# Performance work log

Measured on AMD Instinct MI355X. Metric: run time of the kernel, lower is better.

## Reference

```python
import jax, jax.numpy as jnp
import numpy as np

N = 1048576      # obstacle points
E = 16           # polytope half-planes
HID = 32         # MLP hidden width
J = 10           # unrolled PDHG steps
TAU = 0.5
SIGMA = 0.5
RES = 0.5        # residual_scale for learned prox


def setup_inputs() -> dict:
    key = jax.random.key(0)
    ks = jax.random.split(key, 8)
    f32 = jnp.float32
    x = jax.random.normal(ks[0], (N, 2), dtype=f32) * 3.0
    # geometry buffers: regular 16-gon half-planes G mu <= h
    ang = np.arange(E) * (2.0 * np.pi / E)
    G = jnp.asarray(np.stack([np.cos(ang), np.sin(ang)], axis=1), dtype=f32)  # [E,2]
    h = jnp.ones((E, 1), dtype=f32)
    # encoder: Linear(2->HID), Linear(HID->HID)
    W1 = jax.random.normal(ks[1], (2, HID), dtype=f32) * 0.5
    b1 = jnp.zeros((HID,), dtype=f32)
    W2 = jax.random.normal(ks[2], (HID, HID), dtype=f32) * 0.2
    b2 = jnp.zeros((HID,), dtype=f32)
    # init_mu: Linear(HID->E); init_y: Linear(HID->2)
    Wmu = jax.random.normal(ks[3], (HID, E), dtype=f32) * 0.2
    bmu = jnp.zeros((E,), dtype=f32)
    Wy = jax.random.normal(ks[4], (HID, 2), dtype=f32) * 0.2
    by = jnp.zeros((2,), dtype=f32)
    # prox_head: Linear(2->HID) -> ReLU -> Linear(HID->E)
    Wp1 = jax.random.normal(ks[5], (2, HID), dtype=f32) * 0.5
    bp1 = jnp.zeros((HID,), dtype=f32)
    Wp2 = jax.random.normal(ks[6], (HID, E), dtype=f32) * 0.2
    bp2 = jnp.zeros((E,), dtype=f32)
    return dict(x=x, G=G, h=h, W1=W1, b1=b1, W2=W2, b2=b2,
                Wmu=Wmu, bmu=bmu, Wy=Wy, by=by,
                Wp1=Wp1, bp1=bp1, Wp2=Wp2, bp2=bp2)


def reference(x, G, h, W1, b1, W2, b2, Wmu, bmu, Wy, by, Wp1, bp1, Wp2, bp2):
    def project_mu(mu):
        # clamp_min(0), then scale rows so ||mu @ G||_2 <= 1
        mu = jnp.maximum(mu, 0.0)
        vn = jnp.linalg.norm(mu @ G, axis=1, keepdims=True)  # [N,1]
        return mu / jnp.maximum(vn, 1.0)

    feats = jax.nn.relu(x @ W1 + b1)
    feats = jax.nn.relu(feats @ W2 + b2)
    mu = jax.nn.relu(feats @ Wmu + bmu)          # [N,E]
    y = jnp.tanh(feats @ Wy + by)                # [N,2]
    a_row = x @ G.T - h.T                        # [N,E], constant across steps

    def step(carry, _):
        y, mu = carry
        # dual ascent + unit-ball projection on y
        y = y + SIGMA * (mu @ G)
        y = y / jnp.maximum(jnp.linalg.norm(y, axis=1, keepdims=True), 1.0)
        # primal update on mu
        mu = mu + TAU * (a_row - y @ G.T)
        # learned prox correction
        z = mu @ G                                # [N,2]
        delta = jax.nn.relu(z @ Wp1 + bp1) @ Wp2 + bp2
        mu = project_mu(mu + RES * delta)
        return (y, mu), None

    (y, mu), _ = jax.lax.scan(step, (y, mu), None, length=J)
    return project_mu(mu)
```

## Files before the change

kernel.cpp:

```cpp
#include <hip/hip_runtime.h>

#define E 16
#define HID 32
#define NSTEP 10
#define TAU 0.5f
#define SIGMA 0.5f
#define RES 0.5f
#define NT 4
#define STRIDE 36

typedef __attribute__((ext_vector_type(8))) short bf16x8;
typedef __attribute__((ext_vector_type(4))) float f32x4;
typedef __attribute__((ext_vector_type(4))) unsigned int u32x4;

__device__ __forceinline__ f32x4 mfma16(bf16x8 a, bf16x8 b, f32x4 c) {
    return __builtin_amdgcn_mfma_f32_16x16x32_bf16(a, b, c, 0, 0, 0);
}
__device__ __forceinline__ unsigned int pk2(float lo, float hi) {
    unsigned int r;
    asm("v_cvt_pk_bf16_f32 %0, %1, %2" : "=v"(r) : "v"(lo), "v"(hi));
    return r;
}
__device__ __forceinline__ void split8(const float v[8], bf16x8& hi, bf16x8& lo) {
    u32x4 H, L;
#pragma unroll
    for (int j = 0; j < 4; ++j) {
        const unsigned int h = pk2(v[2 * j], v[2 * j + 1]);
        H[j] = h;
        const float h0 = __uint_as_float(h << 16);
        const float h1 = __uint_as_float(h & 0xffff0000u);
        L[j] = pk2(v[2 * j] - h0, v[2 * j + 1] - h1);
    }
    hi = __builtin_bit_cast(bf16x8, H);
    lo = __builtin_bit_cast(bf16x8, L);
}

__device__ __forceinline__ float fast_tanh(float v) {
    float e = __expf(2.0f * v);
    return 1.0f - __fdividef(2.0f, e + 1.0f);
}
__device__ __forceinline__ float inv_norm_clamped(float n2) {
    return fminf(__builtin_amdgcn_rsqf(n2), 1.0f);
}
__device__ __forceinline__ float bsum4(float x) {
    x += __shfl_xor(x, 16);
    x += __shfl_xor(x, 32);
    return x;
}

__global__ __attribute__((amdgpu_waves_per_eu(3, 4))) __launch_bounds__(256)
void pdhg_kernel(
    const float* __restrict__ xg,  const float* __restrict__ Gg,  const float* __restrict__ hg,
    const float* __restrict__ W1,  const float* __restrict__ b1,
    const float* __restrict__ W2,  const float* __restrict__ b2,
    const float* __restrict__ Wmu, const float* __restrict__ bmu,
    const float* __restrict__ Wy,  const float* __restrict__ by,
    const float* __restrict__ Wp1, const float* __restrict__ bp1,
    const float* __restrict__ Wp2, const float* __restrict__ bp2,
    float* __restrict__ out, int npts)
{
    __shared__ __align__(16) float sT[256 * STRIDE];
    const int tid = threadIdx.x;

    {
        const int pt = blockIdx.x * 256 + tid;
        const int ptc = min(pt, npts - 1);
        const float2 xv = reinterpret_cast<const float2*>(xg)[ptc];
        const float x0 = xv.x, x1 = xv.y;

        float g[HID];
        #pragma unroll
        for (int j = 0; j < HID; ++j) g[j] = b2[j];
        #pragma unroll
        for (int ci = 0; ci < 4; ++ci) {
            float fc[8];
            #pragma unroll
            for (int jj = 0; jj < 8; ++jj) {
                const int j = ci * 8 + jj;
                fc[jj] = fmaxf(fmaf(x0, W1[j], fmaf(x1, W1[HID + j], b1[j])), 0.0f);
            }
            #pragma unroll
            for (int ii = 0; ii < 8; ++ii) {
                const int i = ci * 8 + ii;
                #pragma unroll
                for (int j = 0; j < HID; ++j) g[j] = fmaf(fc[ii], W2[i * HID + j], g[j]);
            }
        }
        float* row = sT + tid * STRIDE;
        row[0] = x0; row[1] = x1;
        #pragma unroll
        for (int jq = 0; jq < 8; ++jq) {
            const int j = jq * 4;
            reinterpret_cast<float4*>(row + 4)[jq] = make_float4(
                fmaxf(g[j], 0.f), fmaxf(g[j + 1], 0.f),
                fmaxf(g[j + 2], 0.f), fmaxf(g[j + 3], 0.f));
        }
    }
    __syncthreads();

    const int lane = tid & 63;
    const int colq = lane & 15;
    const int kg   = lane >> 4;
    const int k0   = kg * 8;
    const int e0   = kg * 4;
    const int pbase = blockIdx.x * 256 + (tid >> 6) * 64;

    float gxr[4], gyr[4];
    f32x4 bp2c;
    #pragma unroll
    for (int r = 0; r < 4; ++r) {
        gxr[r] = Gg[2 * (e0 + r)];
        gyr[r] = Gg[2 * (e0 + r) + 1];
        bp2c[r] = bp2[e0 + r];
    }
    float tg00, tg01, tg11;
    {
        float s00 = 0.f, s01 = 0.f, s11 = 0.f;
        #pragma unroll
        for (int r = 0; r < 4; ++r) {
            s00 = fmaf(gxr[r], gxr[r], s00);
            s01 = fmaf(gxr[r], gyr[r], s01);
            s11 = fmaf(gyr[r], gyr[r], s11);
        }
        tg00 = TAU * bsum4(s00);
        tg01 = TAU * bsum4(s01);
        tg11 = TAU * bsum4(s11);
    }

    bf16x8 wp2h, wp2l;
    {
        float w[8];
        #pragma unroll
        for (int i = 0; i < 8; ++i) w[i] = Wp2[(k0 + i) * E + colq];
        split8(w, wp2h, wp2l);
    }
    float wp1a[8], wp1b[8], bp1r[8];
    #pragma unroll
    for (int i = 0; i < 8; ++i) {
        wp1a[i] = Wp1[k0 + i];
        wp1b[i] = Wp1[HID + k0 + i];
        bp1r[i] = bp1[k0 + i];
    }

    float mu[NT][4], ta[NT][4];
    float y0[NT], y1[NT], v0[NT], v1[NT], tc0[NT], tc1[NT];

    {
        bf16x8 wmuh, wmul;
        {
            float w[8];
            #pragma unroll
            for (int i = 0; i < 8; ++i) w[i] = Wmu[(k0 + i) * E + colq];
            split8(w, wmuh, wmul);
        }
        f32x4 bmuc;
        float hr[4];
        #pragma unroll
        for (int r = 0; r < 4; ++r) { bmuc[r] = bmu[e0 + r]; hr[r] = hg[e0 + r]; }
        float wyar[8], wybr[8];
        #pragma unroll
        for (int i = 0; i < 8; ++i) {
            wyar[i] = Wy[(k0 + i) * 2];
            wybr[i] = Wy[(k0 + i) * 2 + 1];
        }
        const float by0 = by[0], by1 = by[1];

        #pragma unroll
        for (int t = 0; t < NT; ++t) {
            const float* prow = sT + (size_t)((tid >> 6) * 64 + t * 16 + colq) * STRIDE;
            const float px0 = prow[0], px1 = prow[1];
            float gf[8];
            #pragma unroll
            for (int i = 0; i < 8; ++i) gf[i] = prow[4 + k0 + i];
            float p0 = 0.f, p1 = 0.f;
            #pragma unroll
            for (int i = 0; i < 8; ++i) {
                p0 = fmaf(gf[i], wyar[i], p0);
                p1 = fmaf(gf[i], wybr[i], p1);
            }
            y0[t] = fast_tanh(by0 + bsum4(p0));
            y1[t] = fast_tanh(by1 + bsum4(p1));
            bf16x8 gh, gl;
            split8(gf, gh, gl);
            f32x4 d = mfma16(wmul, gh, bmuc);
            d = mfma16(wmuh, gl, d);
            d = mfma16(wmuh, gh, d);
            float q0 = 0.f, q1 = 0.f, r0 = 0.f, r1 = 0.f;
            #pragma unroll
            for (int r = 0; r < 4; ++r) {
                const float m = fmaxf(d[r], 0.0f);
                mu[t][r] = m;
                const float tae = TAU * fmaf(px0, gxr[r], fmaf(px1, gyr[r], -hr[r]));
                ta[t][r] = tae;
                q0 = fmaf(tae, gxr[r], q0);
                q1 = fmaf(tae, gyr[r], q1);
                r0 = fmaf(m, gxr[r], r0);
                r1 = fmaf(m, gyr[r], r1);
            }
            tc0[t] = bsum4(q0); tc1[t] = bsum4(q1);
            v0[t]  = bsum4(r0); v1[t]  = bsum4(r1);
        }
    }

    #pragma unroll 1
    for (int s = 0; s < NSTEP; ++s) {
        #pragma unroll
        for (int t = 0; t < NT; ++t) {
            float a0 = fmaf(SIGMA, v0[t], y0[t]);
            float a1 = fmaf(SIGMA, v1[t], y1[t]);
            const float sc = inv_norm_clamped(fmaf(a0, a0, a1 * a1));
            a0 *= sc; a1 *= sc;
            y0[t] = a0; y1[t] = a1;
            const float z0 = fmaf(-tg00, a0, fmaf(-tg01, a1, v0[t] + tc0[t]));
            const float z1 = fmaf(-tg01, a0, fmaf(-tg11, a1, v1[t] + tc1[t]));
            const float yt0 = TAU * a0, yt1 = TAU * a1;
            #pragma unroll
            for (int r = 0; r < 4; ++r)
                mu[t][r] = fmaf(-yt1, gyr[r], fmaf(-yt0, gxr[r], mu[t][r] + ta[t][r]));
            float hk[8];
            #pragma unroll
            for (int i = 0; i < 8; ++i)
                hk[i] = fmaxf(fmaf(z0, wp1a[i], fmaf(z1, wp1b[i], bp1r[i])), 0.0f);
            bf16x8 bh, bl;
            split8(hk, bh, bl);
            f32x4 d = mfma16(wp2l, bh, bp2c);
            d = mfma16(wp2h, bl, d);
            d = mfma16(wp2h, bh, d);
            float p0 = 0.f, p1 = 0.f;
            #pragma unroll
            for (int r = 0; r < 4; ++r) {
                const float m = fmaxf(fmaf(RES, d[r], mu[t][r]), 0.0f);
                mu[t][r] = m;
                p0 = fmaf(m, gxr[r], p0);
                p1 = fmaf(m, gyr[r], p1);
            }
            p0 = bsum4(p0); p1 = bsum4(p1);
            const float sp = inv_norm_clamped(fmaf(p0, p0, p1 * p1));
            #pragma unroll
            for (int r = 0; r < 4; ++r) mu[t][r] *= sp;
            v0[t] = sp * p0;
            v1[t] = sp * p1;
        }
    }

    #pragma unroll
    for (int t = 0; t < NT; ++t) {
        const int q = pbase + t * 16 + colq;
        if (q < npts)
            *reinterpret_cast<float4*>(out + (size_t)q * E + e0) =
                make_float4(mu[t][0], mu[t][1], mu[t][2], mu[t][3]);
    }
}

extern "C" void kernel_launch(void* const* d_in, const int* in_sizes, int n_in,
                              void* d_out, int out_size, void* d_ws, size_t ws_size,
                              hipStream_t stream) {
    const float* x   = (const float*)d_in[0];
    const float* G   = (const float*)d_in[1];
    const float* h   = (const float*)d_in[2];
    const float* W1  = (const float*)d_in[3];
    const float* b1  = (const float*)d_in[4];
    const float* W2  = (const float*)d_in[5];
    const float* b2  = (const float*)d_in[6];
    const float* Wmu = (const float*)d_in[7];
    const float* bmu = (const float*)d_in[8];
    const float* Wy  = (const float*)d_in[9];
    const float* by  = (const float*)d_in[10];
    const float* Wp1 = (const float*)d_in[11];
    const float* bp1 = (const float*)d_in[12];
    const float* Wp2 = (const float*)d_in[13];
    const float* bp2 = (const float*)d_in[14];

    const int npts = in_sizes[0] / 2;
    const int block = 256;
    const int grid = (npts + block - 1) / block;

    pdhg_kernel<<<grid, block, 0, stream>>>(x, G, h, W1, b1, W2, b2, Wmu, bmu,
                                            Wy, by, Wp1, bp1, Wp2, bp2,
                                            (float*)d_out, npts);
}
```

Measured before the change: 242.5 us.

## Switch prox and init MLPs to 32x32x16 MFMA with two 32-point tiles per wave

Replaces the 16x16x32 bf16 MFMA tiling (four 16-point tiles per wave) with 32x32x16 MFMA on two 32-point tiles. Each lane now holds 8 half-plane outputs, so cross-lane reductions need one shuffle instead of two. The per-element a_row buffer is replaced by a recomputation from TAU*x and TAU*h to save registers. Half of the 32-wide MFMA output rows are padding because E=16, which wastes MFMA work, and the occupancy hint is lowered to 2-3 waves per EU.

```diff
diff --git a/kernel.cpp b/kernel.cpp
--- a/kernel.cpp
+++ b/kernel.cpp
@@ -6,15 +6,15 @@
 #define TAU 0.5f
 #define SIGMA 0.5f
 #define RES 0.5f
-#define NT 4
+#define NT2 2
 #define STRIDE 36
 
 typedef __attribute__((ext_vector_type(8))) short bf16x8;
-typedef __attribute__((ext_vector_type(4))) float f32x4;
+typedef __attribute__((ext_vector_type(16))) float f32x16;
 typedef __attribute__((ext_vector_type(4))) unsigned int u32x4;
 
-__device__ __forceinline__ f32x4 mfma16(bf16x8 a, bf16x8 b, f32x4 c) {
-    return __builtin_amdgcn_mfma_f32_16x16x32_bf16(a, b, c, 0, 0, 0);
+__device__ __forceinline__ f32x16 mfma32(bf16x8 a, bf16x8 b, f32x16 c) {
+    return __builtin_amdgcn_mfma_f32_32x32x16_bf16(a, b, c, 0, 0, 0);
 }
 __device__ __forceinline__ unsigned int pk2(float lo, float hi) {
     unsigned int r;
@@ -42,13 +42,9 @@
 __device__ __forceinline__ float inv_norm_clamped(float n2) {
     return fminf(__builtin_amdgcn_rsqf(n2), 1.0f);
 }
-__device__ __forceinline__ float bsum4(float x) {
-    x += __shfl_xor(x, 16);
-    x += __shfl_xor(x, 32);
-    return x;
-}
-
-__global__ __attribute__((amdgpu_waves_per_eu(3, 4))) __launch_bounds__(256)
+__device__ __forceinline__ float bsum2(float x) { return x + __shfl_xor(x, 32); }
+
+__global__ __attribute__((amdgpu_waves_per_eu(2, 3))) __launch_bounds__(256)
 void pdhg_kernel(
     const float* __restrict__ xg,  const float* __restrict__ Gg,  const float* __restrict__ hg,
     const float* __restrict__ W1,  const float* __restrict__ b1,
@@ -99,113 +95,146 @@
     __syncthreads();
 
     const int lane = tid & 63;
-    const int colq = lane & 15;
-    const int kg   = lane >> 4;
-    const int k0   = kg * 8;
-    const int e0   = kg * 4;
+    const int col  = lane & 31;
+    const int kh   = lane >> 5;
+    const bool colOK = col < E;
+    const int colc = colOK ? col : 0;
     const int pbase = blockIdx.x * 256 + (tid >> 6) * 64;
 
-    float gxr[4], gyr[4];
-    f32x4 bp2c;
-    #pragma unroll
-    for (int r = 0; r < 4; ++r) {
-        gxr[r] = Gg[2 * (e0 + r)];
-        gyr[r] = Gg[2 * (e0 + r) + 1];
-        bp2c[r] = bp2[e0 + r];
-    }
+    float gxr[8], gyr[8], thr8[8];
+    f32x16 cinit;
+    #pragma unroll
+    for (int r = 0; r < 8; ++r) {
+        const int e = (r & 3) + 8 * (r >> 2) + 4 * kh;
+        gxr[r] = Gg[2 * e];
+        gyr[r] = Gg[2 * e + 1];
+        thr8[r] = TAU * hg[e];
+        cinit[r] = bp2[e];
+    }
+    #pragma unroll
+    for (int r = 8; r < 16; ++r) cinit[r] = 0.0f;
+
     float tg00, tg01, tg11;
     {
         float s00 = 0.f, s01 = 0.f, s11 = 0.f;
         #pragma unroll
-        for (int r = 0; r < 4; ++r) {
+        for (int r = 0; r < 8; ++r) {
             s00 = fmaf(gxr[r], gxr[r], s00);
             s01 = fmaf(gxr[r], gyr[r], s01);
             s11 = fmaf(gyr[r], gyr[r], s11);
         }
-        tg00 = TAU * bsum4(s00);
-        tg01 = TAU * bsum4(s01);
-        tg11 = TAU * bsum4(s11);
-    }
-
-    bf16x8 wp2h, wp2l;
+        tg00 = TAU * bsum2(s00);
+        tg01 = TAU * bsum2(s01);
+        tg11 = TAU * bsum2(s11);
+    }
+
+    bf16x8 wp2h[2], wp2l[2];
+    #pragma unroll
+    for (int w = 0; w < 2; ++w) {
+        float wv[8];
+        #pragma unroll
+        for (int i = 0; i < 8; ++i) {
+            const int k = w * 16 + kh * 8 + i;
+            wv[i] = colOK ? Wp2[k * E + colc] : 0.0f;
+        }
+        split8(wv, wp2h[w], wp2l[w]);
+    }
+    float wp1a[16], wp1b[16], bp1r[16];
+    #pragma unroll
+    for (int w = 0; w < 2; ++w)
+        #pragma unroll
+        for (int i = 0; i < 8; ++i) {
+            const int k = w * 16 + kh * 8 + i;
+            wp1a[w * 8 + i] = Wp1[k];
+            wp1b[w * 8 + i] = Wp1[HID + k];
+            bp1r[w * 8 + i] = bp1[k];
+        }
+
+    float mu[NT2][8];
+    float y0[NT2], y1[NT2], v0[NT2], v1[NT2], tc0[NT2], tc1[NT2];
+    float tpx0[NT2], tpx1[NT2];
+
     {
-        float w[8];
-        #pragma unroll
-        for (int i = 0; i < 8; ++i) w[i] = Wp2[(k0 + i) * E + colq];
-        split8(w, wp2h, wp2l);
-    }
-    float wp1a[8], wp1b[8], bp1r[8];
-    #pragma unroll
-    for (int i = 0; i < 8; ++i) {
-        wp1a[i] = Wp1[k0 + i];
-        wp1b[i] = Wp1[HID + k0 + i];
-        bp1r[i] = bp1[k0 + i];
-    }
-
-    float mu[NT][4], ta[NT][4];
-    float y0[NT], y1[NT], v0[NT], v1[NT], tc0[NT], tc1[NT];
-
-    {
-        bf16x8 wmuh, wmul;
-        {
-            float w[8];
-            #pragma unroll
-            for (int i = 0; i < 8; ++i) w[i] = Wmu[(k0 + i) * E + colq];
-            split8(w, wmuh, wmul);
-        }
-        f32x4 bmuc;
-        float hr[4];
-        #pragma unroll
-        for (int r = 0; r < 4; ++r) { bmuc[r] = bmu[e0 + r]; hr[r] = hg[e0 + r]; }
-        float wyar[8], wybr[8];
-        #pragma unroll
-        for (int i = 0; i < 8; ++i) {
-            wyar[i] = Wy[(k0 + i) * 2];
-            wybr[i] = Wy[(k0 + i) * 2 + 1];
-        }
+        bf16x8 wmuh[2], wmul[2];
+        #pragma unroll
+        for (int w = 0; w < 2; ++w) {
+            float wv[8];
+            #pragma unroll
+            for (int i = 0; i < 8; ++i) {
+                const int k = w * 16 + kh * 8 + i;
+                wv[i] = colOK ? Wmu[k * E + colc] : 0.0f;
+            }
+            split8(wv, wmuh[w], wmul[w]);
+        }
+        float wya[16], wyb[16];
+        #pragma unroll
+        for (int w = 0; w < 2; ++w)
+            #pragma unroll
+            for (int i = 0; i < 8; ++i) {
+                const int k = w * 16 + kh * 8 + i;
+                wya[w * 8 + i] = Wy[k * 2];
+                wyb[w * 8 + i] = Wy[k * 2 + 1];
+            }
+        f32x16 cinitH;
+        #pragma unroll
+        for (int r = 0; r < 8; ++r)
+            cinitH[r] = bmu[(r & 3) + 8 * (r >> 2) + 4 * kh];
+        #pragma unroll
+        for (int r = 8; r < 16; ++r) cinitH[r] = 0.0f;
         const float by0 = by[0], by1 = by[1];
 
         #pragma unroll
-        for (int t = 0; t < NT; ++t) {
-            const float* prow = sT + (size_t)((tid >> 6) * 64 + t * 16 + colq) * STRIDE;
+        for (int t = 0; t < NT2; ++t) {
+            const float* prow = sT + (size_t)((tid >> 6) * 64 + t * 32 + col) * STRIDE;
+            const float4* p4 = reinterpret_cast<const float4*>(prow);
+            float gA[8], gB[8];
+            {
+                const float4 a0 = p4[1 + 2 * kh], a1 = p4[2 + 2 * kh];
+                const float4 b0 = p4[5 + 2 * kh], b1v = p4[6 + 2 * kh];
+                gA[0]=a0.x; gA[1]=a0.y; gA[2]=a0.z; gA[3]=a0.w;
+                gA[4]=a1.x; gA[5]=a1.y; gA[6]=a1.z; gA[7]=a1.w;
+                gB[0]=b0.x; gB[1]=b0.y; gB[2]=b0.z; gB[3]=b0.w;
+                gB[4]=b1v.x; gB[5]=b1v.y; gB[6]=b1v.z; gB[7]=b1v.w;
+            }
             const float px0 = prow[0], px1 = prow[1];
-            float gf[8];
-            #pragma unroll
-            for (int i = 0; i < 8; ++i) gf[i] = prow[4 + k0 + i];
             float p0 = 0.f, p1 = 0.f;
             #pragma unroll
             for (int i = 0; i < 8; ++i) {
-                p0 = fmaf(gf[i], wyar[i], p0);
-                p1 = fmaf(gf[i], wybr[i], p1);
-            }
-            y0[t] = fast_tanh(by0 + bsum4(p0));
-            y1[t] = fast_tanh(by1 + bsum4(p1));
-            bf16x8 gh, gl;
-            split8(gf, gh, gl);
-            f32x4 d = mfma16(wmul, gh, bmuc);
-            d = mfma16(wmuh, gl, d);
-            d = mfma16(wmuh, gh, d);
+                p0 = fmaf(gA[i], wya[i], p0);      p1 = fmaf(gA[i], wyb[i], p1);
+                p0 = fmaf(gB[i], wya[8 + i], p0);  p1 = fmaf(gB[i], wyb[8 + i], p1);
+            }
+            y0[t] = fast_tanh(by0 + bsum2(p0));
+            y1[t] = fast_tanh(by1 + bsum2(p1));
+            bf16x8 ghA, glA, ghB, glB;
+            split8(gA, ghA, glA);
+            split8(gB, ghB, glB);
+            f32x16 d = mfma32(wmul[0], ghA, cinitH);
+            d = mfma32(wmuh[0], glA, d);
+            d = mfma32(wmuh[0], ghA, d);
+            d = mfma32(wmul[1], ghB, d);
+            d = mfma32(wmuh[1], glB, d);
+            d = mfma32(wmuh[1], ghB, d);
             float q0 = 0.f, q1 = 0.f, r0 = 0.f, r1 = 0.f;
             #pragma unroll
-            for (int r = 0; r < 4; ++r) {
+            for (int r = 0; r < 8; ++r) {
                 const float m = fmaxf(d[r], 0.0f);
                 mu[t][r] = m;
-                const float tae = TAU * fmaf(px0, gxr[r], fmaf(px1, gyr[r], -hr[r]));
-                ta[t][r] = tae;
+                const float tae = fmaf(TAU, fmaf(px0, gxr[r], px1 * gyr[r]), -thr8[r]);
                 q0 = fmaf(tae, gxr[r], q0);
                 q1 = fmaf(tae, gyr[r], q1);
                 r0 = fmaf(m, gxr[r], r0);
                 r1 = fmaf(m, gyr[r], r1);
             }
-            tc0[t] = bsum4(q0); tc1[t] = bsum4(q1);
-            v0[t]  = bsum4(r0); v1[t]  = bsum4(r1);
+            tc0[t] = bsum2(q0); tc1[t] = bsum2(q1);
+            v0[t]  = bsum2(r0); v1[t]  = bsum2(r1);
+            tpx0[t] = TAU * px0; tpx1[t] = TAU * px1;
         }
     }
 
     #pragma unroll 1
     for (int s = 0; s < NSTEP; ++s) {
         #pragma unroll
-        for (int t = 0; t < NT; ++t) {
+        for (int t = 0; t < NT2; ++t) {
             float a0 = fmaf(SIGMA, v0[t], y0[t]);
             float a1 = fmaf(SIGMA, v1[t], y1[t]);
             const float sc = inv_norm_clamped(fmaf(a0, a0, a1 * a1));
@@ -213,42 +242,63 @@
             y0[t] = a0; y1[t] = a1;
             const float z0 = fmaf(-tg00, a0, fmaf(-tg01, a1, v0[t] + tc0[t]));
             const float z1 = fmaf(-tg01, a0, fmaf(-tg11, a1, v1[t] + tc1[t]));
-            const float yt0 = TAU * a0, yt1 = TAU * a1;
-            #pragma unroll
-            for (int r = 0; r < 4; ++r)
-                mu[t][r] = fmaf(-yt1, gyr[r], fmaf(-yt0, gxr[r], mu[t][r] + ta[t][r]));
-            float hk[8];
-            #pragma unroll
-            for (int i = 0; i < 8; ++i)
-                hk[i] = fmaxf(fmaf(z0, wp1a[i], fmaf(z1, wp1b[i], bp1r[i])), 0.0f);
-            bf16x8 bh, bl;
-            split8(hk, bh, bl);
-            f32x4 d = mfma16(wp2l, bh, bp2c);
-            d = mfma16(wp2h, bl, d);
-            d = mfma16(wp2h, bh, d);
+            const float u0 = fmaf(-TAU, a0, tpx0[t]);
+            const float u1 = fmaf(-TAU, a1, tpx1[t]);
+            #pragma unroll
+            for (int r = 0; r < 8; ++r)
+                mu[t][r] = fmaf(u1, gyr[r], fmaf(u0, gxr[r], mu[t][r] - thr8[r]));
+
+            f32x16 d;
+            {
+                float hk[8];
+                #pragma unroll
+                for (int i = 0; i < 8; ++i)
+                    hk[i] = fmaxf(fmaf(z0, wp1a[i], fmaf(z1, wp1b[i], bp1r[i])), 0.0f);
+                bf16x8 bh, bl;
+                split8(hk, bh, bl);
+                d = mfma32(wp2l[0], bh, cinit);
+                d = mfma32(wp2h[0], bl, d);
+                d = mfma32(wp2h[0], bh, d);
+            }
+            {
+                float hk[8];
+                #pragma unroll
+                for (int i = 0; i < 8; ++i)
+                    hk[i] = fmaxf(fmaf(z0, wp1a[8 + i], fmaf(z1, wp1b[8 + i], bp1r[8 + i])), 0.0f);
+                bf16x8 bh, bl;
+                split8(hk, bh, bl);
+                d = mfma32(wp2l[1], bh, d);
+                d = mfma32(wp2h[1], bl, d);
+                d = mfma32(wp2h[1], bh, d);
+            }
+
             float p0 = 0.f, p1 = 0.f;
             #pragma unroll
-            for (int r = 0; r < 4; ++r) {
+            for (int r = 0; r < 8; ++r) {
                 const float m = fmaxf(fmaf(RES, d[r], mu[t][r]), 0.0f);
                 mu[t][r] = m;
                 p0 = fmaf(m, gxr[r], p0);
                 p1 = fmaf(m, gyr[r], p1);
             }
-            p0 = bsum4(p0); p1 = bsum4(p1);
+            p0 = bsum2(p0); p1 = bsum2(p1);
             const float sp = inv_norm_clamped(fmaf(p0, p0, p1 * p1));
             #pragma unroll
-            for (int r = 0; r < 4; ++r) mu[t][r] *= sp;
+            for (int r = 0; r < 8; ++r) mu[t][r] *= sp;
             v0[t] = sp * p0;
             v1[t] = sp * p1;
         }
     }
 
     #pragma unroll
-    for (int t = 0; t < NT; ++t) {
-        const int q = pbase + t * 16 + colq;
-        if (q < npts)
-            *reinterpret_cast<float4*>(out + (size_t)q * E + e0) =
+    for (int t = 0; t < NT2; ++t) {
+        const int q = pbase + t * 32 + col;
+        if (q < npts) {
+            float* o = out + (size_t)q * E;
+            *reinterpret_cast<float4*>(o + 4 * kh) =
                 make_float4(mu[t][0], mu[t][1], mu[t][2], mu[t][3]);
+            *reinterpret_cast<float4*>(o + 8 + 4 * kh) =
+                make_float4(mu[t][4], mu[t][5], mu[t][6], mu[t][7]);
+        }
     }
 }
 
```

Measured after the change: 248.3 us. 1.02x slower.
